# Optimization experiments

Measured on AMD Instinct MI355X. Metric: run time of the kernel, lower is better.

The kernel has to match this reference:

```python
import jax, jax.numpy as jnp
import numpy as np

PRECISION_WEIGHT = 3.0
FALSE_POSITIVE_PENALTY = 5.0
BATCH = 8388608
NUM_CLASSES = 2

def setup_inputs() -> dict:
    key = jax.random.key(0)
    k1, k2 = jax.random.split(key)
    logits = jax.random.normal(k1, (BATCH, NUM_CLASSES), dtype=jnp.float32)
    targets = jax.random.randint(k2, (BATCH,), 0, NUM_CLASSES, dtype=jnp.int64 if jax.config.jax_enable_x64 else jnp.int32)
    return {"logits": logits, "targets": targets}

def reference(logits, targets):
    # per-sample cross entropy: -log_softmax(logits)[target]
    logp = jax.nn.log_softmax(logits, axis=1)                     # (B, C)
    ce_loss = -jnp.take_along_axis(logp, targets[:, None].astype(jnp.int32), axis=1)[:, 0]  # (B,)
    preds = jnp.argmax(logits, axis=1)                            # (B,)
    t = targets.astype(jnp.int32)
    p = preds.astype(jnp.int32)
    # false negative (t==1, p==0) -> 1.0 ; false positive (t==0, p==1) -> 5.0 ; else 0.1
    penalty = jnp.where((t == 1) & (p == 0), 1.0,
              jnp.where((t == 0) & (p == 1), FALSE_POSITIVE_PENALTY, 0.1)).astype(logits.dtype)
    weighted = ce_loss * (1.0 + PRECISION_WEIGHT * penalty)
    return jnp.mean(weighted)
```

## Files before the change

kernel.cpp:

```cpp
#include <hip/hip_runtime.h>
#include <math.h>


#define LOSS_BATCH 8388608
#define LOSS_GRID  2048
#define LOSS_BLOCK 256

__device__ __forceinline__ float sample_loss(float l0, float l1, int t) {
    float m   = fmaxf(l0, l1);
    float d   = fabsf(l0 - l1);
    float lse = m + log1pf(__expf(-d));
    float ce  = lse - (t ? l1 : l0);
    bool p1 = l1 > l0;
    float w;
    if (t == 1 && !p1)      w = 4.0f;
    else if (t == 0 && p1)  w = 16.0f;
    else                    w = 1.3f;
    return ce * w;
}

__global__ __launch_bounds__(LOSS_BLOCK) void loss_partial_kernel(
        const float4* __restrict__ logits4,
        const int4*   __restrict__ tgt4,
        float*        __restrict__ partials)
{
    const int nquads = LOSS_BATCH / 4;
    float acc = 0.0f;
    for (int q = blockIdx.x * blockDim.x + threadIdx.x; q < nquads;
         q += gridDim.x * blockDim.x) {
        float4 a = logits4[2 * q];
        float4 b = logits4[2 * q + 1];
        int4   t = tgt4[q];
        acc += sample_loss(a.x, a.y, t.x);
        acc += sample_loss(a.z, a.w, t.y);
        acc += sample_loss(b.x, b.y, t.z);
        acc += sample_loss(b.z, b.w, t.w);
    }
    #pragma unroll
    for (int off = 32; off > 0; off >>= 1)
        acc += __shfl_down(acc, off, 64);
    __shared__ float smem[LOSS_BLOCK / 64];
    int lane = threadIdx.x & 63;
    int wid  = threadIdx.x >> 6;
    if (lane == 0) smem[wid] = acc;
    __syncthreads();
    if (threadIdx.x == 0) {
        float s = 0.0f;
        #pragma unroll
        for (int i = 0; i < LOSS_BLOCK / 64; ++i) s += smem[i];
        partials[blockIdx.x] = s;
    }
}

__global__ __launch_bounds__(256) void loss_final_kernel(
        const float* __restrict__ partials, float* __restrict__ out)
{
    double acc = 0.0;
    for (int i = threadIdx.x; i < LOSS_GRID; i += blockDim.x)
        acc += (double)partials[i];
    #pragma unroll
    for (int off = 32; off > 0; off >>= 1)
        acc += __shfl_down(acc, off, 64);
    __shared__ double smem[4];
    int lane = threadIdx.x & 63;
    int wid  = threadIdx.x >> 6;
    if (lane == 0) smem[wid] = acc;
    __syncthreads();
    if (threadIdx.x == 0) {
        double s = smem[0] + smem[1] + smem[2] + smem[3];
        out[0] = (float)(s / (double)LOSS_BATCH);
    }
}

extern "C" void kernel_launch(void* const* d_in, const int* in_sizes, int n_in,
                              void* d_out, int out_size, void* d_ws, size_t ws_size,
                              hipStream_t stream) {
    const float4* logits4 = (const float4*)d_in[0];
    const int4*   tgt4    = (const int4*)d_in[1];
    float* partials = (float*)d_ws;
    float* out      = (float*)d_out;

    loss_partial_kernel<<<LOSS_GRID, LOSS_BLOCK, 0, stream>>>(logits4, tgt4, partials);
    loss_final_kernel<<<1, 256, 0, stream>>>(partials, out);
}
```

Before: 119.7 us.

## Fully unroll loads into registers with nontemporal vector loads, cheaper math

Replaces the grid-stride loop with a fixed, fully unrolled set of iterations per thread. All logits and targets loads are issued up front as nontemporal vector loads (float4 logits, int2 targets), then the computation runs over the registers, so each thread has more memory requests in flight. It also switches log1pf to the fast __logf and simplifies the penalty-weight selection. The cost is higher register pressure, slightly lower precision in the log term, and code that assumes the batch divides evenly across the grid.

Result: no change. 120.3 us (+0.5%).

```diff
diff --git a/kernel.cpp b/kernel.cpp
--- a/kernel.cpp
+++ b/kernel.cpp
@@ -5,37 +5,47 @@
 #define LOSS_BATCH 8388608
 #define LOSS_GRID  2048
 #define LOSS_BLOCK 256
+#define LOSS_THREADS (LOSS_GRID * LOSS_BLOCK)
+#define LOSS_NF4     (LOSS_BATCH / 2)
+#define LOSS_ITERS   (LOSS_NF4 / LOSS_THREADS)
+
+typedef float fvec4 __attribute__((ext_vector_type(4)));
+typedef int   ivec2 __attribute__((ext_vector_type(2)));
 
 __device__ __forceinline__ float sample_loss(float l0, float l1, int t) {
     float m   = fmaxf(l0, l1);
     float d   = fabsf(l0 - l1);
-    float lse = m + log1pf(__expf(-d));
+    float lse = m + __logf(1.0f + __expf(-d));
     float ce  = lse - (t ? l1 : l0);
-    bool p1 = l1 > l0;
-    float w;
-    if (t == 1 && !p1)      w = 4.0f;
-    else if (t == 0 && p1)  w = 16.0f;
-    else                    w = 1.3f;
+    int p1 = (l1 > l0) ? 1 : 0;
+    float w = 1.3f;
+    if (t != p1) w = t ? 4.0f : 16.0f;
     return ce * w;
 }
 
 __global__ __launch_bounds__(LOSS_BLOCK) void loss_partial_kernel(
-        const float4* __restrict__ logits4,
-        const int4*   __restrict__ tgt4,
-        float*        __restrict__ partials)
+        const fvec4* __restrict__ logits4,
+        const ivec2* __restrict__ tgt2,
+        float*       __restrict__ partials)
 {
-    const int nquads = LOSS_BATCH / 4;
+    const int tid = blockIdx.x * LOSS_BLOCK + threadIdx.x;
+
+    fvec4 L[LOSS_ITERS];
+    ivec2 T[LOSS_ITERS];
+    #pragma unroll
+    for (int j = 0; j < LOSS_ITERS; ++j) {
+        int idx = j * LOSS_THREADS + tid;
+        L[j] = __builtin_nontemporal_load(&logits4[idx]);
+        T[j] = __builtin_nontemporal_load(&tgt2[idx]);
+    }
+
     float acc = 0.0f;
-    for (int q = blockIdx.x * blockDim.x + threadIdx.x; q < nquads;
-         q += gridDim.x * blockDim.x) {
-        float4 a = logits4[2 * q];
-        float4 b = logits4[2 * q + 1];
-        int4   t = tgt4[q];
-        acc += sample_loss(a.x, a.y, t.x);
-        acc += sample_loss(a.z, a.w, t.y);
-        acc += sample_loss(b.x, b.y, t.z);
-        acc += sample_loss(b.z, b.w, t.w);
+    #pragma unroll
+    for (int j = 0; j < LOSS_ITERS; ++j) {
+        acc += sample_loss(L[j].x, L[j].y, T[j].x);
+        acc += sample_loss(L[j].z, L[j].w, T[j].y);
     }
+
     #pragma unroll
     for (int off = 32; off > 0; off >>= 1)
         acc += __shfl_down(acc, off, 64);
@@ -75,11 +85,11 @@
 extern "C" void kernel_launch(void* const* d_in, const int* in_sizes, int n_in,
                               void* d_out, int out_size, void* d_ws, size_t ws_size,
                               hipStream_t stream) {
-    const float4* logits4 = (const float4*)d_in[0];
-    const int4*   tgt4    = (const int4*)d_in[1];
+    const fvec4* logits4 = (const fvec4*)d_in[0];
+    const ivec2* tgt2    = (const ivec2*)d_in[1];
     float* partials = (float*)d_ws;
     float* out      = (float*)d_out;
 
-    loss_partial_kernel<<<LOSS_GRID, LOSS_BLOCK, 0, stream>>>(logits4, tgt4, partials);
+    loss_partial_kernel<<<LOSS_GRID, LOSS_BLOCK, 0, stream>>>(logits4, tgt2, partials);
     loss_final_kernel<<<1, 256, 0, stream>>>(partials, out);
 }
```
